# Kernel optimization log

Hardware: AMD Instinct MI355X
Metric: run time of the kernel (lower is better)

## Reference

```python
import jax, jax.numpy as jnp
import numpy as np

B, C, D, H, K = 512, 112, 128, 8, 8  # batch, channels(=seq), d_model, heads, conv kernel
HD = D // H
SCALE = HD ** -0.5
BN_EPS = 1e-5
LN_EPS = 1e-5


def setup_inputs() -> dict:
    key = jax.random.key(0)
    ks = jax.random.split(key, 12)
    s = 0.05
    return {
        "x": jax.random.normal(ks[0], (B, C, D), jnp.float32),
        "conv_w": jax.random.normal(ks[1], (C, 1, K), jnp.float32) * s,
        "conv_b": jax.random.normal(ks[2], (C,), jnp.float32) * s,
        "bn_g": jnp.ones((C,), jnp.float32),
        "bn_b": jnp.zeros((C,), jnp.float32),
        "bn_m": jnp.zeros((C,), jnp.float32),
        "bn_v": jnp.ones((C,), jnp.float32),
        "wq": jax.random.normal(ks[3], (D, D), jnp.float32) * s,
        "bq": jax.random.normal(ks[4], (D,), jnp.float32) * s,
        "wk": jax.random.normal(ks[5], (D, D), jnp.float32) * s,
        "bk": jax.random.normal(ks[6], (D,), jnp.float32) * s,
        "wv": jax.random.normal(ks[7], (D, D), jnp.float32) * s,
        "bv": jax.random.normal(ks[8], (D,), jnp.float32) * s,
        "wo": jax.random.normal(ks[9], (D, D), jnp.float32) * s,
        "bo": jax.random.normal(ks[10], (D,), jnp.float32) * s,
        "ln_g": jnp.ones((D,), jnp.float32),
        "ln_b": jnp.zeros((D,), jnp.float32),
    }


def _forward(x, conv_w, conv_b, bn_g, bn_b, bn_m, bn_v,
             wq, bq, wk, bk, wv, bv, wo, bo, ln_g, ln_b):
    # resnet_1: depthwise Conv1d(padding='same', k=8) -> GELU -> BatchNorm1d (eval)
    # torch 'same' padding for even k: left = (k-1)//2 = 3, right = 4
    h = jax.lax.conv_general_dilated(
        x, conv_w, window_strides=(1,), padding=[(3, 4)],
        dimension_numbers=("NCH", "OIH", "NCH"), feature_group_count=C)
    h = h + conv_b[None, :, None]
    h = jax.nn.gelu(h, approximate=False)
    h = (h - bn_m[None, :, None]) * (bn_g[None, :, None] * jax.lax.rsqrt(bn_v + BN_EPS)[None, :, None]) + bn_b[None, :, None]
    src = x + h  # [B, C, D]; attention treats C as sequence dim

    # multi-head attention (hand-rolled, res_attention path with prev=None)
    q = (src @ wq.T + bq).reshape(B, C, H, HD).transpose(0, 2, 1, 3)  # [B,H,S,hd]
    k = (src @ wk.T + bk).reshape(B, C, H, HD).transpose(0, 2, 1, 3)
    v = (src @ wv.T + bv).reshape(B, C, H, HD).transpose(0, 2, 1, 3)
    scores = jnp.einsum("bhqd,bhkd->bhqk", q, k) * SCALE  # [B,H,S,S]
    attn = jax.nn.softmax(scores, axis=-1)
    out = jnp.einsum("bhqk,bhkd->bhqd", attn, v)  # [B,H,S,hd]
    out = out.transpose(0, 2, 1, 3).reshape(B, C, D)
    out = out @ wo.T + bo

    # residual + LayerNorm over last dim
    src = src + out
    mu = jnp.mean(src, axis=-1, keepdims=True)
    var = jnp.mean(jnp.square(src - mu), axis=-1, keepdims=True)
    src = (src - mu) * jax.lax.rsqrt(var + LN_EPS) * ln_g + ln_b
    return src


def reference(x, conv_w, conv_b, bn_g, bn_b, bn_m, bn_v,
              wq, bq, wk, bk, wv, bv, wo, bo, ln_g, ln_b):
    return _forward(x, conv_w, conv_b, bn_g, bn_b, bn_m, bn_v,
                    wq, bq, wk, bk, wv, bv, wo, bo, ln_g, ln_b)
```

## Files before the change

kernel.cpp:

```cpp
#include <hip/hip_runtime.h>
#include <hip/hip_bf16.h>

#define BB 512
#define CC 112
#define DD 128
#define HH 8
#define HD 16
#define KK 8
#define QS 1792

typedef unsigned short u16;
typedef short short8 __attribute__((ext_vector_type(8)));
typedef float f32x4 __attribute__((ext_vector_type(4)));
typedef float f32x16 __attribute__((ext_vector_type(16)));

#define MFMA16(a, b, c) __builtin_amdgcn_mfma_f32_16x16x32_bf16(a, b, c, 0, 0, 0)
#define MFMA32(a, b, c) __builtin_amdgcn_mfma_f32_32x32x16_bf16(a, b, c, 0, 0, 0)

__device__ inline u16 f2bf(float f) {
  union { float f; unsigned u; } v{f};
  unsigned r = (v.u + 0x7FFFu + ((v.u >> 16) & 1u)) >> 16;
  return (u16)r;
}
__device__ inline float bf2f(u16 u) {
  union { unsigned u; float f; } v;
  v.u = ((unsigned)u) << 16;
  return v.f;
}
__device__ inline unsigned pk2(float a, float b) {
  __hip_bfloat162 h = __float22bfloat162_rn(float2{a, b});
  union { __hip_bfloat162 h; unsigned u; } v{h};
  return v.u;
}

__device__ inline unsigned permx32(unsigned x) {
  unsigned a = x, b = x;
  asm("v_permlane32_swap_b32 %0, %1" : "+v"(a), "+v"(b));
  return (threadIdx.x & 32) ? a : b;
}
__device__ inline float permx32f(float x) {
  union { float f; unsigned u; } v{x};
  v.u = permx32(v.u);
  return v.f;
}

__global__ __launch_bounds__(512, 4) void k_conv(
    const float* __restrict__ x, const float* __restrict__ cw,
    const float* __restrict__ cb, const float* __restrict__ bg,
    const float* __restrict__ bb_, const float* __restrict__ bm,
    const float* __restrict__ bv, const float* __restrict__ wq,
    const float* __restrict__ wk, const float* __restrict__ wv,
    const float* __restrict__ wo, u16* __restrict__ src_b,
    u16* __restrict__ w_b) {
  const int b = blockIdx.x;
  const int t = threadIdx.x;
  const int tg = t >> 2, sub = t & 3;
  if (tg < CC) {
    const int row = tg, ch = tg;
    const float4 w0 = *(const float4*)(cw + ch * KK);
    const float4 w1 = *(const float4*)(cw + ch * KK + 4);
    const float cbv = cb[ch];
    const float bscale = bg[ch] * rsqrtf(bv[ch] + 1e-5f);
    const float bmv = bm[ch], bbv = bb_[ch];
    const float* __restrict__ xr = x + ((size_t)b * CC + row) * DD;
    float in[40];
#pragma unroll
    for (int f = 0; f < 10; ++f) {
      const int fi = 8 * sub - 1 + f;
      float4 vv = {0.f, 0.f, 0.f, 0.f};
      if (fi >= 0 && fi < 32) vv = ((const float4*)xr)[fi];
      in[f * 4 + 0] = vv.x; in[f * 4 + 1] = vv.y;
      in[f * 4 + 2] = vv.z; in[f * 4 + 3] = vv.w;
    }
    unsigned pkv[16];
#pragma unroll
    for (int i2 = 0; i2 < 16; ++i2) {
      float oo[2];
#pragma unroll
      for (int j = 0; j < 2; ++j) {
        const int i = i2 * 2 + j;
        float a = 0.f;
        a = fmaf(in[i + 1], w0.x, a);
        a = fmaf(in[i + 2], w0.y, a);
        a = fmaf(in[i + 3], w0.z, a);
        a = fmaf(in[i + 4], w0.w, a);
        a = fmaf(in[i + 5], w1.x, a);
        a = fmaf(in[i + 6], w1.y, a);
        a = fmaf(in[i + 7], w1.z, a);
        a = fmaf(in[i + 8], w1.w, a);
        a += cbv;
        const float u = fmaf(0.044715f * a, a, 1.0f);
        const float e = __expf(a * u * -1.5957691216f);
        const float g2 = a * __frcp_rn(1.f + e);
        oo[j] = in[i + 4] + (g2 - bmv) * bscale + bbv;
      }
      pkv[i2] = pk2(oo[0], oo[1]);
    }
    uint4* gsr = (uint4*)(src_b + ((size_t)b * CC + row) * DD + sub * 32);
#pragma unroll
    for (int k4 = 0; k4 < 4; ++k4) gsr[k4] = ((uint4*)pkv)[k4];
  } else if (t >= 448) {
    const int p = b * 64 + (t - 448);
    const int sel = p >> 13, off = p & 8191;
    const float* w = (sel == 0) ? wq : (sel == 1) ? wk : (sel == 2) ? wv : wo;
    const float2 v = ((const float2*)w)[off];
    ((unsigned*)w_b)[p] = pk2(v.x, v.y);
  }
}

__global__ __launch_bounds__(512, 4) void k_main(
    const u16* __restrict__ src_b, const u16* __restrict__ w_b,
    const float* __restrict__ bq, const float* __restrict__ bk,
    const float* __restrict__ bvv, const float* __restrict__ bo,
    const float* __restrict__ lg, const float* __restrict__ lb,
    float* __restrict__ out) {
  __shared__ __attribute__((aligned(16))) u16 QO[HH * CC * HD];
  __shared__ __attribute__((aligned(16))) u16 KL[HH * CC * HD];
  const int b = blockIdx.x;
  const int t = threadIdx.x;
  const int wave = t >> 6, lane = t & 63;
  const int h = wave;
  const int quad = lane >> 4, n = lane & 15;

  unsigned pv[14];
  {
    short8 Wq[4], Wk[4], Wv[4];
#pragma unroll
    for (int kf = 0; kf < 4; ++kf) {
      const int wi = (h * 16 + n) * DD + kf * 32 + quad * 8;
      Wq[kf] = *(const short8*)(w_b + wi);
      Wk[kf] = *(const short8*)(w_b + 16384 + wi);
      Wv[kf] = *(const short8*)(w_b + 32768 + wi);
    }
    const float bqv = bq[h * 16 + n];
    const float bkv = bk[h * 16 + n];
    const float bvv2 = bvv[h * 16 + n];
    u16* qoh = QO + h * QS;
    u16* klh = KL + h * QS;
    const u16* __restrict__ sp = src_b + (size_t)b * CC * DD;
#pragma unroll
    for (int mt = 0; mt < 7; ++mt) {
      short8 A[4];
#pragma unroll
      for (int kf = 0; kf < 4; ++kf)
        A[kf] = *(const short8*)(sp + (mt * 16 + n) * DD + kf * 32 + quad * 8);
      f32x4 aq = {0.f, 0.f, 0.f, 0.f};
      f32x4 ak = {0.f, 0.f, 0.f, 0.f};
      f32x4 av = {0.f, 0.f, 0.f, 0.f};
#pragma unroll
      for (int kf = 0; kf < 4; ++kf) {
        aq = MFMA16(A[kf], Wq[kf], aq);
        ak = MFMA16(A[kf], Wk[kf], ak);
        av = MFMA16(A[kf], Wv[kf], av);
      }
      const int row0 = mt * 16 + quad * 4;
#pragma unroll
      for (int r = 0; r < 4; ++r) {
        qoh[(row0 + r) * HD + n] = f2bf(aq[r] + bqv);
        klh[(row0 + r) * HD + n] = f2bf(ak[r] + bkv);
      }
      pv[2 * mt] = pk2(av[0] + bvv2, av[1] + bvv2);
      pv[2 * mt + 1] = pk2(av[2] + bvv2, av[3] + bvv2);
    }
  }

  {
    const int lo = lane & 31, hi = lane >> 5, hi8 = hi * 8;
    u16* qoh = QO + h * QS;
    const u16* klh = KL + h * QS;
    const float C1 = 0.25f * 1.44269504088896341f;
    unsigned pvp[14];
#pragma unroll
    for (int j = 0; j < 14; ++j) pvp[j] = __shfl_xor(pv[j], 16);
    for (int qt = 0; qt < 4; ++qt) {
      const int qt0 = qt * 32;
      short8 Bq = {};
      if (qt0 + lo < CC) Bq = *(const short8*)(qoh + (qt0 + lo) * HD + hi8);
      float sp4[4] = {0.f, 0.f, 0.f, 0.f};
      f32x16 oacc = {};
#pragma unroll
      for (int mt = 0; mt < 4; ++mt) {
        short8 Ak = {};
        const int key = mt * 32 + lo;
        if (key < CC) Ak = *(const short8*)(klh + key * HD + hi8);
        f32x16 z = {};
        f32x16 sa = MFMA32(Ak, Bq, z);
        const int rmax = (mt == 3) ? 8 : 16;
        float pf[16];
#pragma unroll
        for (int r = 0; r < 16; ++r)
          if (r < rmax) {
            const float p = exp2f(sa[r] * C1);
            pf[r] = p;
            sp4[r & 3] += p;
          }
        unsigned U0[4], U1[4];
        const int rqmax = (mt == 3) ? 2 : 4;
#pragma unroll
        for (int rq = 0; rq < 4; ++rq)
          if (rq < rqmax) {
            U0[rq] = pk2(pf[4 * rq + 0], pf[4 * rq + 1]);
            U1[rq] = pk2(pf[4 * rq + 2], pf[4 * rq + 3]);
          }
        const int kkmax = (mt == 3) ? 1 : 2;
#pragma unroll
        for (int kk = 0; kk < 2; ++kk)
          if (kk < kkmax) {
            const int kt = 2 * mt + kk;
            const int c = 2 * kk;
            const unsigned own0 = hi ? U0[c + 1] : U0[c];
            const unsigned own1 = hi ? U1[c + 1] : U1[c];
            const unsigned snd0 = hi ? U0[c] : U0[c + 1];
            const unsigned snd1 = hi ? U1[c] : U1[c + 1];
            const unsigned got0 = permx32(snd0);
            const unsigned got1 = permx32(snd1);
            union { unsigned u[4]; short8 s; } ap;
            ap.u[0] = hi ? got0 : own0;
            ap.u[1] = hi ? got1 : own1;
            ap.u[2] = hi ? own0 : got0;
            ap.u[3] = hi ? own1 : got1;
            union { unsigned u[4]; short8 s; } bvf;
            bvf.u[0] = pv[2 * kt];
            bvf.u[1] = pv[2 * kt + 1];
            bvf.u[2] = pvp[2 * kt];
            bvf.u[3] = pvp[2 * kt + 1];
            oacc = MFMA32(ap.s, bvf.s, oacc);
          }
      }
      float sum = (sp4[0] + sp4[1]) + (sp4[2] + sp4[3]);
      sum += permx32f(sum);
      const float rinv = 1.f / sum;
#pragma unroll
      for (int r = 0; r < 16; ++r) {
        const int rr = (r & 3) + 8 * (r >> 2) + 4 * hi;
        const float rv = __shfl(rinv, rr);
        if (lo < HD && qt0 + rr < CC)
          qoh[(qt0 + rr) * HD + lo] = f2bf(oacc[r] * rv);
      }
    }
  }
  __syncthreads();

  if (wave < 7) {
    const int mt = wave;
    const u16* __restrict__ w_bo = w_b + 3 * 16384;
    short8 A[4];
#pragma unroll
    for (int kf = 0; kf < 4; ++kf) {
      const int head = 2 * kf + (quad >> 1);
      A[kf] =
          *(const short8*)&QO[head * QS + (mt * 16 + n) * HD + (quad & 1) * 8];
    }
    float v[8][4];
#pragma unroll
    for (int nt = 0; nt < 8; ++nt) {
      f32x4 acc = {0.f, 0.f, 0.f, 0.f};
#pragma unroll
      for (int kf = 0; kf < 4; ++kf) {
        const short8 Bf =
            *(const short8*)(w_bo + (nt * 16 + n) * DD + kf * 32 + quad * 8);
        acc = MFMA16(A[kf], Bf, acc);
      }
      const int col = nt * 16 + n;
      const float bcol = bo[col];
#pragma unroll
      for (int r = 0; r < 4; ++r)
        v[nt][r] =
            acc[r] + bcol +
            bf2f(src_b[((size_t)b * CC + mt * 16 + quad * 4 + r) * DD + col]);
    }
    float sum[4] = {0.f, 0.f, 0.f, 0.f}, sq[4] = {0.f, 0.f, 0.f, 0.f};
#pragma unroll
    for (int nt = 0; nt < 8; ++nt)
#pragma unroll
      for (int r = 0; r < 4; ++r) {
        sum[r] += v[nt][r];
        sq[r] = fmaf(v[nt][r], v[nt][r], sq[r]);
      }
#pragma unroll
    for (int d = 1; d < 16; d <<= 1)
#pragma unroll
      for (int r = 0; r < 4; ++r) {
        sum[r] += __shfl_xor(sum[r], d);
        sq[r] += __shfl_xor(sq[r], d);
      }
    float mu[4], rs[4];
#pragma unroll
    for (int r = 0; r < 4; ++r) {
      mu[r] = sum[r] * (1.f / DD);
      const float var = sq[r] * (1.f / DD) - mu[r] * mu[r];
      rs[r] = rsqrtf(var + 1e-5f);
    }
#pragma unroll
    for (int nt = 0; nt < 8; ++nt) {
      const int col = nt * 16 + n;
      const float g = lg[col], be = lb[col];
#pragma unroll
      for (int r = 0; r < 4; ++r)
        out[((size_t)b * CC + mt * 16 + quad * 4 + r) * DD + col] =
            (v[nt][r] - mu[r]) * rs[r] * g + be;
    }
  }
}

extern "C" void kernel_launch(void* const* d_in, const int* in_sizes, int n_in,
                              void* d_out, int out_size, void* d_ws,
                              size_t ws_size, hipStream_t stream) {
  (void)in_sizes; (void)n_in; (void)out_size; (void)ws_size;
  const float* x   = (const float*)d_in[0];
  const float* cw  = (const float*)d_in[1];
  const float* cb  = (const float*)d_in[2];
  const float* bg  = (const float*)d_in[3];
  const float* bb  = (const float*)d_in[4];
  const float* bm  = (const float*)d_in[5];
  const float* bv  = (const float*)d_in[6];
  const float* wq  = (const float*)d_in[7];
  const float* bq  = (const float*)d_in[8];
  const float* wk  = (const float*)d_in[9];
  const float* bk  = (const float*)d_in[10];
  const float* wv  = (const float*)d_in[11];
  const float* bvv = (const float*)d_in[12];
  const float* wo  = (const float*)d_in[13];
  const float* bo  = (const float*)d_in[14];
  const float* lg  = (const float*)d_in[15];
  const float* lb  = (const float*)d_in[16];
  float* out = (float*)d_out;

  const size_t NE = (size_t)BB * CC * DD;
  u16* ub = (u16*)d_ws;
  u16* src_b = ub;
  u16* w_b   = ub + NE;

  k_conv<<<BB, 512, 0, stream>>>(x, cw, cb, bg, bb, bm, bv, wq, wk, wv, wo,
                                 src_b, w_b);
  k_main<<<BB, 512, 0, stream>>>(src_b, w_b, bq, bk, bvv, bo, lg, lb, out);
}
```

Baseline: 173.3 us.

## Fuse conv and attention kernels into one launch, convert weights to bf16 in-register

Merges the conv/GELU/BN kernel and the attention+LayerNorm kernel into a single kernel separated by a block barrier. The separate bf16 weight-conversion pass is dropped, and each wave now loads fp32 weights and packs them to bf16 in registers. The QKV projection is split into a Q/K pass and a separate V pass, so fewer weight fragments are live at once. This removes one kernel launch and the weight-staging buffer, at the cost of redundant fp32 weight loads and conversions in every block. The src tile still goes through global memory between the two phases, relying on the barrier and caches for visibility.

```diff
diff --git a/kernel.cpp b/kernel.cpp
--- a/kernel.cpp
+++ b/kernel.cpp
@@ -44,75 +44,27 @@
   return v.f;
 }
 
-__global__ __launch_bounds__(512, 4) void k_conv(
+__device__ inline short8 ldw8(const float* __restrict__ p) {
+  const float4 a = *(const float4*)p;
+  const float4 c = *(const float4*)(p + 4);
+  union { unsigned u[4]; short8 s; } r;
+  r.u[0] = pk2(a.x, a.y);
+  r.u[1] = pk2(a.z, a.w);
+  r.u[2] = pk2(c.x, c.y);
+  r.u[3] = pk2(c.z, c.w);
+  return r.s;
+}
+
+__global__ __launch_bounds__(512, 4) void k_all(
     const float* __restrict__ x, const float* __restrict__ cw,
     const float* __restrict__ cb, const float* __restrict__ bg,
     const float* __restrict__ bb_, const float* __restrict__ bm,
     const float* __restrict__ bv, const float* __restrict__ wq,
-    const float* __restrict__ wk, const float* __restrict__ wv,
-    const float* __restrict__ wo, u16* __restrict__ src_b,
-    u16* __restrict__ w_b) {
-  const int b = blockIdx.x;
-  const int t = threadIdx.x;
-  const int tg = t >> 2, sub = t & 3;
-  if (tg < CC) {
-    const int row = tg, ch = tg;
-    const float4 w0 = *(const float4*)(cw + ch * KK);
-    const float4 w1 = *(const float4*)(cw + ch * KK + 4);
-    const float cbv = cb[ch];
-    const float bscale = bg[ch] * rsqrtf(bv[ch] + 1e-5f);
-    const float bmv = bm[ch], bbv = bb_[ch];
-    const float* __restrict__ xr = x + ((size_t)b * CC + row) * DD;
-    float in[40];
-#pragma unroll
-    for (int f = 0; f < 10; ++f) {
-      const int fi = 8 * sub - 1 + f;
-      float4 vv = {0.f, 0.f, 0.f, 0.f};
-      if (fi >= 0 && fi < 32) vv = ((const float4*)xr)[fi];
-      in[f * 4 + 0] = vv.x; in[f * 4 + 1] = vv.y;
-      in[f * 4 + 2] = vv.z; in[f * 4 + 3] = vv.w;
-    }
-    unsigned pkv[16];
-#pragma unroll
-    for (int i2 = 0; i2 < 16; ++i2) {
-      float oo[2];
-#pragma unroll
-      for (int j = 0; j < 2; ++j) {
-        const int i = i2 * 2 + j;
-        float a = 0.f;
-        a = fmaf(in[i + 1], w0.x, a);
-        a = fmaf(in[i + 2], w0.y, a);
-        a = fmaf(in[i + 3], w0.z, a);
-        a = fmaf(in[i + 4], w0.w, a);
-        a = fmaf(in[i + 5], w1.x, a);
-        a = fmaf(in[i + 6], w1.y, a);
-        a = fmaf(in[i + 7], w1.z, a);
-        a = fmaf(in[i + 8], w1.w, a);
-        a += cbv;
-        const float u = fmaf(0.044715f * a, a, 1.0f);
-        const float e = __expf(a * u * -1.5957691216f);
-        const float g2 = a * __frcp_rn(1.f + e);
-        oo[j] = in[i + 4] + (g2 - bmv) * bscale + bbv;
-      }
-      pkv[i2] = pk2(oo[0], oo[1]);
-    }
-    uint4* gsr = (uint4*)(src_b + ((size_t)b * CC + row) * DD + sub * 32);
-#pragma unroll
-    for (int k4 = 0; k4 < 4; ++k4) gsr[k4] = ((uint4*)pkv)[k4];
-  } else if (t >= 448) {
-    const int p = b * 64 + (t - 448);
-    const int sel = p >> 13, off = p & 8191;
-    const float* w = (sel == 0) ? wq : (sel == 1) ? wk : (sel == 2) ? wv : wo;
-    const float2 v = ((const float2*)w)[off];
-    ((unsigned*)w_b)[p] = pk2(v.x, v.y);
-  }
-}
-
-__global__ __launch_bounds__(512, 4) void k_main(
-    const u16* __restrict__ src_b, const u16* __restrict__ w_b,
-    const float* __restrict__ bq, const float* __restrict__ bk,
-    const float* __restrict__ bvv, const float* __restrict__ bo,
-    const float* __restrict__ lg, const float* __restrict__ lb,
+    const float* __restrict__ bq, const float* __restrict__ wk,
+    const float* __restrict__ bk, const float* __restrict__ wv,
+    const float* __restrict__ bvv, const float* __restrict__ wo,
+    const float* __restrict__ bo, const float* __restrict__ lg,
+    const float* __restrict__ lb, u16* __restrict__ src_b,
     float* __restrict__ out) {
   __shared__ __attribute__((aligned(16))) u16 QO[HH * CC * HD];
   __shared__ __attribute__((aligned(16))) u16 KL[HH * CC * HD];
@@ -122,45 +74,111 @@
   const int h = wave;
   const int quad = lane >> 4, n = lane & 15;
 
+  {
+    const int tg = t >> 2, sub = t & 3;
+    if (tg < CC) {
+      const int row = tg, ch = tg;
+      const float4 w0 = *(const float4*)(cw + ch * KK);
+      const float4 w1 = *(const float4*)(cw + ch * KK + 4);
+      const float cbv = cb[ch];
+      const float bscale = bg[ch] * rsqrtf(bv[ch] + 1e-5f);
+      const float bmv = bm[ch], bbv = bb_[ch];
+      const float* __restrict__ xr = x + ((size_t)b * CC + row) * DD;
+      float in[40];
+#pragma unroll
+      for (int f = 0; f < 10; ++f) {
+        const int fi = 8 * sub - 1 + f;
+        float4 vv = {0.f, 0.f, 0.f, 0.f};
+        if (fi >= 0 && fi < 32) vv = ((const float4*)xr)[fi];
+        in[f * 4 + 0] = vv.x; in[f * 4 + 1] = vv.y;
+        in[f * 4 + 2] = vv.z; in[f * 4 + 3] = vv.w;
+      }
+      unsigned pkv[16];
+#pragma unroll
+      for (int i2 = 0; i2 < 16; ++i2) {
+        float oo[2];
+#pragma unroll
+        for (int j = 0; j < 2; ++j) {
+          const int i = i2 * 2 + j;
+          float a = 0.f;
+          a = fmaf(in[i + 1], w0.x, a);
+          a = fmaf(in[i + 2], w0.y, a);
+          a = fmaf(in[i + 3], w0.z, a);
+          a = fmaf(in[i + 4], w0.w, a);
+          a = fmaf(in[i + 5], w1.x, a);
+          a = fmaf(in[i + 6], w1.y, a);
+          a = fmaf(in[i + 7], w1.z, a);
+          a = fmaf(in[i + 8], w1.w, a);
+          a += cbv;
+          const float u = fmaf(0.044715f * a, a, 1.0f);
+          const float e = __expf(a * u * -1.5957691216f);
+          const float g2 = a * __frcp_rn(1.f + e);
+          oo[j] = in[i + 4] + (g2 - bmv) * bscale + bbv;
+        }
+        pkv[i2] = pk2(oo[0], oo[1]);
+      }
+      uint4* gsr = (uint4*)(src_b + ((size_t)b * CC + row) * DD + sub * 32);
+#pragma unroll
+      for (int k4 = 0; k4 < 4; ++k4) gsr[k4] = ((uint4*)pkv)[k4];
+    }
+  }
+  __syncthreads();
+
   unsigned pv[14];
   {
-    short8 Wq[4], Wk[4], Wv[4];
-#pragma unroll
-    for (int kf = 0; kf < 4; ++kf) {
-      const int wi = (h * 16 + n) * DD + kf * 32 + quad * 8;
-      Wq[kf] = *(const short8*)(w_b + wi);
-      Wk[kf] = *(const short8*)(w_b + 16384 + wi);
-      Wv[kf] = *(const short8*)(w_b + 32768 + wi);
-    }
-    const float bqv = bq[h * 16 + n];
-    const float bkv = bk[h * 16 + n];
-    const float bvv2 = bvv[h * 16 + n];
     u16* qoh = QO + h * QS;
     u16* klh = KL + h * QS;
     const u16* __restrict__ sp = src_b + (size_t)b * CC * DD;
-#pragma unroll
-    for (int mt = 0; mt < 7; ++mt) {
-      short8 A[4];
-#pragma unroll
-      for (int kf = 0; kf < 4; ++kf)
-        A[kf] = *(const short8*)(sp + (mt * 16 + n) * DD + kf * 32 + quad * 8);
-      f32x4 aq = {0.f, 0.f, 0.f, 0.f};
-      f32x4 ak = {0.f, 0.f, 0.f, 0.f};
-      f32x4 av = {0.f, 0.f, 0.f, 0.f};
+    const int woff = (h * 16 + n) * DD + quad * 8;
+    {
+      short8 Wq[4], Wk[4];
 #pragma unroll
       for (int kf = 0; kf < 4; ++kf) {
-        aq = MFMA16(A[kf], Wq[kf], aq);
-        ak = MFMA16(A[kf], Wk[kf], ak);
-        av = MFMA16(A[kf], Wv[kf], av);
-      }
-      const int row0 = mt * 16 + quad * 4;
-#pragma unroll
-      for (int r = 0; r < 4; ++r) {
-        qoh[(row0 + r) * HD + n] = f2bf(aq[r] + bqv);
-        klh[(row0 + r) * HD + n] = f2bf(ak[r] + bkv);
-      }
-      pv[2 * mt] = pk2(av[0] + bvv2, av[1] + bvv2);
-      pv[2 * mt + 1] = pk2(av[2] + bvv2, av[3] + bvv2);
+        Wq[kf] = ldw8(wq + woff + kf * 32);
+        Wk[kf] = ldw8(wk + woff + kf * 32);
+      }
+      const float bqv = bq[h * 16 + n];
+      const float bkv = bk[h * 16 + n];
+#pragma unroll
+      for (int mt = 0; mt < 7; ++mt) {
+        short8 A[4];
+#pragma unroll
+        for (int kf = 0; kf < 4; ++kf)
+          A[kf] =
+              *(const short8*)(sp + (mt * 16 + n) * DD + kf * 32 + quad * 8);
+        f32x4 aq = {0.f, 0.f, 0.f, 0.f};
+        f32x4 ak = {0.f, 0.f, 0.f, 0.f};
+#pragma unroll
+        for (int kf = 0; kf < 4; ++kf) {
+          aq = MFMA16(A[kf], Wq[kf], aq);
+          ak = MFMA16(A[kf], Wk[kf], ak);
+        }
+        const int row0 = mt * 16 + quad * 4;
+#pragma unroll
+        for (int r = 0; r < 4; ++r) {
+          qoh[(row0 + r) * HD + n] = f2bf(aq[r] + bqv);
+          klh[(row0 + r) * HD + n] = f2bf(ak[r] + bkv);
+        }
+      }
+    }
+    {
+      short8 Wv[4];
+#pragma unroll
+      for (int kf = 0; kf < 4; ++kf) Wv[kf] = ldw8(wv + woff + kf * 32);
+      const float bvv2 = bvv[h * 16 + n];
+#pragma unroll
+      for (int mt = 0; mt < 7; ++mt) {
+        short8 A[4];
+#pragma unroll
+        for (int kf = 0; kf < 4; ++kf)
+          A[kf] =
+              *(const short8*)(sp + (mt * 16 + n) * DD + kf * 32 + quad * 8);
+        f32x4 av = {0.f, 0.f, 0.f, 0.f};
+#pragma unroll
+        for (int kf = 0; kf < 4; ++kf) av = MFMA16(A[kf], Wv[kf], av);
+        pv[2 * mt] = pk2(av[0] + bvv2, av[1] + bvv2);
+        pv[2 * mt + 1] = pk2(av[2] + bvv2, av[3] + bvv2);
+      }
     }
   }
 
@@ -243,7 +261,6 @@
 
   if (wave < 7) {
     const int mt = wave;
-    const u16* __restrict__ w_bo = w_b + 3 * 16384;
     short8 A[4];
 #pragma unroll
     for (int kf = 0; kf < 4; ++kf) {
@@ -257,8 +274,7 @@
       f32x4 acc = {0.f, 0.f, 0.f, 0.f};
 #pragma unroll
       for (int kf = 0; kf < 4; ++kf) {
-        const short8 Bf =
-            *(const short8*)(w_bo + (nt * 16 + n) * DD + kf * 32 + quad * 8);
+        const short8 Bf = ldw8(wo + (nt * 16 + n) * DD + kf * 32 + quad * 8);
         acc = MFMA16(A[kf], Bf, acc);
       }
       const int col = nt * 16 + n;
@@ -326,12 +342,8 @@
   const float* lb  = (const float*)d_in[16];
   float* out = (float*)d_out;
 
-  const size_t NE = (size_t)BB * CC * DD;
-  u16* ub = (u16*)d_ws;
-  u16* src_b = ub;
-  u16* w_b   = ub + NE;
-
-  k_conv<<<BB, 512, 0, stream>>>(x, cw, cb, bg, bb, bm, bv, wq, wk, wv, wo,
-                                 src_b, w_b);
-  k_main<<<BB, 512, 0, stream>>>(src_b, w_b, bq, bk, bvv, bo, lg, lb, out);
-}
+  u16* src_b = (u16*)d_ws;
+
+  k_all<<<BB, 512, 0, stream>>>(x, cw, cb, bg, bb, bm, bv, wq, bq, wk, bk,
+                                wv, bvv, wo, bo, lg, lb, src_b, out);
+}
```

After: 185.9 us. +7.3%, slower.
